# Performance work log

Measured on AMD Instinct MI355X. Metric: run time of the kernel, lower is better.

## Reference

```python
import jax, jax.numpy as jnp
import numpy as np


def setup_inputs() -> dict:
    key = jax.random.key(0)
    k1, k2 = jax.random.split(key)
    # positive inputs -> positive matmul outputs, so log is well-defined
    x = jax.random.uniform(k1, (8, 2048, 1024), dtype=jnp.float32)
    matrix = jax.random.uniform(k2, (1024, 1024), dtype=jnp.float32)
    return {"x": x, "matrix": matrix}


def reference(x, matrix):
    # mm_big: shifted quantized matmul; mm_small: no-shift quantized matmul.
    # In float math both compute the same product (quantization differs only
    # in fixed-point scaling), so we compute it once; XLA would CSE anyway.
    y_big = jnp.einsum('bsk,km->bsm', x, matrix)    # [B,S,M]
    y_small = jnp.einsum('bsk,km->bsm', x, matrix)  # NoShiftMM, same float math

    big = (y_big > 0).astype(x.dtype)   # gt0
    small = 1.0 - big                   # oplus(neg(big)) = 1 + (-big)

    eps = jnp.finfo(x.dtype).tiny
    # AddIdentityTLUT(torch.log): LUT approximation of log; float reference is log.
    z_big = jnp.log(jnp.maximum(y_big, eps)) * big      # lut_big -> mul_big
    z_small = jnp.log(jnp.maximum(y_small, eps)) * small  # lut_small -> mul_small
    return z_big + z_small  # add_output
```

## Files before the change

### kernel.cpp

```cpp
#include <hip/hip_runtime.h>
#include <cstdint>
#include <cstddef>

#define M_GLOB 16384
#define N_GLOB 1024
#define K_GLOB 1024

#define BM 256
#define BN 128
#define BKF 128

typedef unsigned char  u8;
typedef unsigned short u16;
typedef __attribute__((ext_vector_type(4))) float  f32x4;
typedef __attribute__((ext_vector_type(16))) float f32x16;
typedef __attribute__((ext_vector_type(4))) unsigned int  u32x4;
typedef __attribute__((ext_vector_type(2))) unsigned int  u32x2;
typedef __attribute__((ext_vector_type(8))) int  i32x8;
typedef __attribute__((ext_vector_type(8))) __bf16 bf16x8;

typedef const __attribute__((address_space(1))) void* gas1_t;
typedef __attribute__((address_space(3))) void* las3_t;

static __device__ __forceinline__ void load_lds16(const void* g, void* l) {
    __builtin_amdgcn_global_load_lds((gas1_t)g, (las3_t)l, 16, 0, 0);
}

static __device__ __forceinline__ unsigned pack2_bf16(float lo, float hi) {
    unsigned bl = __builtin_bit_cast(unsigned, lo);
    unsigned bh = __builtin_bit_cast(unsigned, hi);
    return (bh & 0xFFFF0000u) | (bl >> 16);
}

static __device__ __forceinline__ unsigned cvt4_fp8(float a, float b, float c, float d) {
    int w = __builtin_amdgcn_cvt_pk_fp8_f32(a, b, 0, false);
    w = __builtin_amdgcn_cvt_pk_fp8_f32(c, d, w, true);
    return (unsigned)w;
}

__global__ __launch_bounds__(256)
void prep_fp8_kernel(const float* __restrict__ A, u8* __restrict__ Ab,
                     const float* __restrict__ B, u8* __restrict__ Bt, int nA) {
    __shared__ float tile[32][33];
    const int tid = threadIdx.x;
    if ((int)blockIdx.x < nA) {
        const size_t i = ((size_t)blockIdx.x * 256 + tid) * 16;
        f32x4 f0 = *(const f32x4*)(A + i);
        f32x4 f1 = *(const f32x4*)(A + i + 4);
        f32x4 f2 = *(const f32x4*)(A + i + 8);
        f32x4 f3 = *(const f32x4*)(A + i + 12);
        u32x4 o;
        o.x = cvt4_fp8(f0.x, f0.y, f0.z, f0.w);
        o.y = cvt4_fp8(f1.x, f1.y, f1.z, f1.w);
        o.z = cvt4_fp8(f2.x, f2.y, f2.z, f2.w);
        o.w = cvt4_fp8(f3.x, f3.y, f3.z, f3.w);
        *(u32x4*)(Ab + i) = o;
    } else {
        const int bid = (int)blockIdx.x - nA;
        const int n0 = (bid & 31) * 32;
        const int k0 = (bid >> 5) * 32;
        const int tx = tid & 31;
        const int ty = tid >> 5;
#pragma unroll
        for (int i = 0; i < 32; i += 8)
            tile[ty + i][tx] = B[(size_t)(k0 + ty + i) * N_GLOB + n0 + tx];
        __syncthreads();
#pragma unroll
        for (int i = 0; i < 32; i += 8) {
            int w = __builtin_amdgcn_cvt_pk_fp8_f32(tile[tx][ty + i], 0.f, 0, false);
            Bt[(size_t)(n0 + ty + i) * K_GLOB + k0 + tx] = (u8)(w & 0xFF);
        }
    }
}

__global__ __launch_bounds__(256, 2)
void gemm_mx_kernel(const u8* __restrict__ A,
                    const u8* __restrict__ Bt,
                    float* __restrict__ C)
{
    __shared__ __attribute__((aligned(16))) char smem[49152];
    float* Cs = (float*)smem;

    const int tid  = threadIdx.x;
    const int wave = tid >> 6;
    const int lane = tid & 63;
    const int wr   = wave >> 1;
    const int wc   = wave & 1;
    const int l32  = lane & 31;
    const int half = lane >> 5;

    const int b    = blockIdx.x;
    const int xcd  = b & 7;
    const int idx  = b >> 3;
    const int m0   = (xcd * 8 + (idx >> 3)) * BM;
    const int n0   = (idx & 7) * BN;

    const int srow = lane >> 3;
    const int sc   = (lane & 7) ^ srow;
    const u8* gA = A  + (size_t)(m0 + srow) * K_GLOB + sc * 16;
    const u8* gB = Bt + (size_t)(n0 + srow) * K_GLOB + sc * 16;

    f32x16 acc[4][2];
#pragma unroll
    for (int i = 0; i < 4; ++i)
#pragma unroll
        for (int j = 0; j < 2; ++j)
#pragma unroll
            for (int r = 0; r < 16; ++r)
                acc[i][j][r] = 0.f;

    const int swz = lane & 7;
    const int scale1 = 0x7F7F7F7F;

    for (int kt = 0; kt < K_GLOB / BKF; ++kt) {
        const size_t k0 = (size_t)kt * BKF;
#pragma unroll
        for (int s = 0; s < 8; ++s) {
            const int rows0 = (s * 4 + wave) * 8;
            load_lds16(gA + (size_t)rows0 * K_GLOB + k0, smem + rows0 * 128);
        }
#pragma unroll
        for (int s = 0; s < 4; ++s) {
            const int rows0 = (s * 4 + wave) * 8;
            load_lds16(gB + (size_t)rows0 * K_GLOB + k0, smem + 32768 + rows0 * 128);
        }
        __syncthreads();

#pragma unroll
        for (int s = 0; s < 2; ++s) {
            const int c0 = s * 4 + half * 2;
            const int p0 = ((c0    ) ^ swz) * 16;
            const int p1 = ((c0 + 1) ^ swz) * 16;
            i32x8 af[4], bf[2];
#pragma unroll
            for (int i = 0; i < 4; ++i) {
                const int row = wr * 128 + i * 32 + l32;
                u32x4 lo = *(const u32x4*)(smem + row * 128 + p0);
                u32x4 hi = *(const u32x4*)(smem + row * 128 + p1);
                af[i][0] = lo.x; af[i][1] = lo.y; af[i][2] = lo.z; af[i][3] = lo.w;
                af[i][4] = hi.x; af[i][5] = hi.y; af[i][6] = hi.z; af[i][7] = hi.w;
            }
#pragma unroll
            for (int j = 0; j < 2; ++j) {
                const int row = wc * 64 + j * 32 + l32;
                u32x4 lo = *(const u32x4*)(smem + 32768 + row * 128 + p0);
                u32x4 hi = *(const u32x4*)(smem + 32768 + row * 128 + p1);
                bf[j][0] = lo.x; bf[j][1] = lo.y; bf[j][2] = lo.z; bf[j][3] = lo.w;
                bf[j][4] = hi.x; bf[j][5] = hi.y; bf[j][6] = hi.z; bf[j][7] = hi.w;
            }
#pragma unroll
            for (int i = 0; i < 4; ++i)
#pragma unroll
                for (int j = 0; j < 2; ++j)
                    acc[i][j] = __builtin_amdgcn_mfma_scale_f32_32x32x64_f8f6f4(
                        af[i], bf[j], acc[i][j],
                        0 , 0 ,
                        0, scale1, 0, scale1);
        }
        __syncthreads();
    }

    const float LN2 = 0.69314718055994530942f;
    const int c4 = tid & 31;
    const int r0 = tid >> 5;
#pragma unroll
    for (int h = 0; h < 4; ++h) {
        __syncthreads();
        if (wr == (h >> 1)) {
#pragma unroll
            for (int ii = 0; ii < 2; ++ii) {
                const int i = (h & 1) * 2 + ii;
#pragma unroll
                for (int j = 0; j < 2; ++j) {
                    const int col = wc * 64 + j * 32 + l32;
#pragma unroll
                    for (int r = 0; r < 16; ++r) {
                        const int row32 = (r & 3) + 8 * (r >> 2) + 4 * half;
                        float v = fmaxf(acc[i][j][r], 1.17549435e-38f);
                        Cs[(ii * 32 + row32) * 132 + col] = __log2f(v) * LN2;
                    }
                }
            }
        }
        __syncthreads();
#pragma unroll
        for (int s2 = 0; s2 < 8; ++s2) {
            const int row = s2 * 8 + r0;
            f32x4 v = *(const f32x4*)&Cs[row * 132 + c4 * 4];
            __builtin_nontemporal_store(v,
                (f32x4*)&C[(size_t)(m0 + h * 64 + row) * N_GLOB + n0 + c4 * 4]);
        }
    }
}

#define FBM 128
#define FBN 128
#define LDK 40
__global__ __launch_bounds__(256)
void logmm_fused_kernel(const float* __restrict__ A,
                        const float* __restrict__ Bf,
                        float* __restrict__ C)
{
    __shared__ u16 As[FBM][LDK];
    __shared__ u16 Bs[FBN][LDK];

    const int tid  = threadIdx.x;
    const int lane = tid & 63;
    const int wave = tid >> 6;
    const int wr   = wave >> 1;
    const int wc   = wave & 1;
    const int quad = lane >> 4;
    const int l16  = lane & 15;

    const int m0 = blockIdx.y * FBM;
    const int n0 = blockIdx.x * FBN;

    f32x4 acc[4][4];
#pragma unroll
    for (int i = 0; i < 4; ++i)
#pragma unroll
        for (int j = 0; j < 4; ++j)
            acc[i][j] = f32x4{0.f, 0.f, 0.f, 0.f};

    const int ga_row = tid >> 2;
    const int ga_c8  = (tid & 3) * 8;
    const int fb_nt = tid >> 3;
    const int fb_kt = tid & 7;

    for (int kt = 0; kt < K_GLOB / 32; ++kt) {
        const int k0 = kt * 32;
#pragma unroll
        for (int s = 0; s < 2; ++s) {
            const int row = ga_row + s * 64;
            const float* src = A + (size_t)(m0 + row) * K_GLOB + k0 + ga_c8;
            f32x4 f0 = *(const f32x4*)src;
            f32x4 f1 = *(const f32x4*)(src + 4);
            u32x4 o;
            o.x = pack2_bf16(f0.x, f0.y);
            o.y = pack2_bf16(f0.z, f0.w);
            o.z = pack2_bf16(f1.x, f1.y);
            o.w = pack2_bf16(f1.z, f1.w);
            *(u32x4*)&As[row][ga_c8] = o;
        }
        {
            f32x4 r0 = *(const f32x4*)(Bf + (size_t)(k0 + fb_kt * 4 + 0) * N_GLOB + n0 + fb_nt * 4);
            f32x4 r1 = *(const f32x4*)(Bf + (size_t)(k0 + fb_kt * 4 + 1) * N_GLOB + n0 + fb_nt * 4);
            f32x4 r2 = *(const f32x4*)(Bf + (size_t)(k0 + fb_kt * 4 + 2) * N_GLOB + n0 + fb_nt * 4);
            f32x4 r3 = *(const f32x4*)(Bf + (size_t)(k0 + fb_kt * 4 + 3) * N_GLOB + n0 + fb_nt * 4);
#pragma unroll
            for (int j = 0; j < 4; ++j) {
                u32x2 o;
                o.x = pack2_bf16(r0[j], r1[j]);
                o.y = pack2_bf16(r2[j], r3[j]);
                *(u32x2*)&Bs[fb_nt * 4 + j][fb_kt * 4] = o;
            }
        }

        __syncthreads();

        bf16x8 af[4], bfr[4];
#pragma unroll
        for (int i = 0; i < 4; ++i)
            af[i] = __builtin_bit_cast(bf16x8, *(const u32x4*)&As[wr * 64 + i * 16 + l16][quad * 8]);
#pragma unroll
        for (int j = 0; j < 4; ++j)
            bfr[j] = __builtin_bit_cast(bf16x8, *(const u32x4*)&Bs[wc * 64 + j * 16 + l16][quad * 8]);

#pragma unroll
        for (int i = 0; i < 4; ++i)
#pragma unroll
            for (int j = 0; j < 4; ++j)
                acc[i][j] = __builtin_amdgcn_mfma_f32_16x16x32_bf16(af[i], bfr[j], acc[i][j], 0, 0, 0);

        __syncthreads();
    }

    const float LN2 = 0.69314718055994530942f;
#pragma unroll
    for (int i = 0; i < 4; ++i) {
#pragma unroll
        for (int j = 0; j < 4; ++j) {
            const int col = n0 + wc * 64 + j * 16 + l16;
#pragma unroll
            for (int r = 0; r < 4; ++r) {
                const int row = m0 + wr * 64 + i * 16 + quad * 4 + r;
                float v = fmaxf(acc[i][j][r], 1.17549435e-38f);
                C[(size_t)row * N_GLOB + col] = __log2f(v) * LN2;
            }
        }
    }
}

extern "C" void kernel_launch(void* const* d_in, const int* in_sizes, int n_in,
                              void* d_out, int out_size, void* d_ws, size_t ws_size,
                              hipStream_t stream) {
    const float* A = (const float*)d_in[0];
    const float* B = (const float*)d_in[1];
    float* C = (float*)d_out;

    const size_t bt_bytes = (size_t)N_GLOB * K_GLOB;
    const size_t ab_bytes = (size_t)M_GLOB * K_GLOB;
    const int nA = (M_GLOB * K_GLOB) / (256 * 16);

    if (ws_size >= bt_bytes + ab_bytes) {
        u8* Bt = (u8*)d_ws;
        u8* Ab = (u8*)d_ws + bt_bytes;
        prep_fp8_kernel<<<nA + 1024, 256, 0, stream>>>(A, Ab, B, Bt, nA);
        gemm_mx_kernel<<<(M_GLOB / BM) * (N_GLOB / BN), 256, 0, stream>>>(Ab, Bt, C);
    } else {
        logmm_fused_kernel<<<dim3(N_GLOB / FBN, M_GLOB / FBM), 256, 0, stream>>>(A, B, C);
    }
}
```

Measured before the change: 132.8 us.

## Prefetch next K tile into registers instead of direct global-to-LDS loads

Replaces the direct global_load_lds copies with register staging: the next K tile is loaded from global memory into registers while the MFMAs for the current tile run, then written to LDS at the top of the next iteration. This is meant to hide global memory latency behind compute, since the old scheme waited on the loads before every tile. The trailing __syncthreads becomes a raw s_barrier with no waitcnt, which relies on the LDS reads having completed before the MFMAs consume them. In exchange it uses more VGPRs for the staging buffers, which may lower occupancy.

```diff
diff --git a/kernel.cpp b/kernel.cpp
--- a/kernel.cpp
+++ b/kernel.cpp
@@ -19,13 +19,6 @@
 typedef __attribute__((ext_vector_type(8))) int  i32x8;
 typedef __attribute__((ext_vector_type(8))) __bf16 bf16x8;
 
-typedef const __attribute__((address_space(1))) void* gas1_t;
-typedef __attribute__((address_space(3))) void* las3_t;
-
-static __device__ __forceinline__ void load_lds16(const void* g, void* l) {
-    __builtin_amdgcn_global_load_lds((gas1_t)g, (las3_t)l, 16, 0, 0);
-}
-
 static __device__ __forceinline__ unsigned pack2_bf16(float lo, float hi) {
     unsigned bl = __builtin_bit_cast(unsigned, lo);
     unsigned bh = __builtin_bit_cast(unsigned, hi);
@@ -36,6 +29,10 @@
     int w = __builtin_amdgcn_cvt_pk_fp8_f32(a, b, 0, false);
     w = __builtin_amdgcn_cvt_pk_fp8_f32(c, d, w, true);
     return (unsigned)w;
+}
+
+static __device__ __forceinline__ void barrier_raw() {
+    asm volatile("s_barrier" ::: "memory");
 }
 
 __global__ __launch_bounds__(256)
@@ -96,7 +93,8 @@
     const int n0   = (idx & 7) * BN;
 
     const int srow = lane >> 3;
-    const int sc   = (lane & 7) ^ srow;
+    const int sp   = lane & 7;
+    const int sc   = sp ^ srow;
     const u8* gA = A  + (size_t)(m0 + srow) * K_GLOB + sc * 16;
     const u8* gB = Bt + (size_t)(n0 + srow) * K_GLOB + sc * 16;
 
@@ -112,19 +110,36 @@
     const int swz = lane & 7;
     const int scale1 = 0x7F7F7F7F;
 
+    u32x4 ra[8], rb[4];
+#pragma unroll
+    for (int s = 0; s < 8; ++s)
+        ra[s] = *(const u32x4*)(gA + (size_t)((s * 4 + wave) * 8) * K_GLOB);
+#pragma unroll
+    for (int s = 0; s < 4; ++s)
+        rb[s] = *(const u32x4*)(gB + (size_t)((s * 4 + wave) * 8) * K_GLOB);
+
     for (int kt = 0; kt < K_GLOB / BKF; ++kt) {
-        const size_t k0 = (size_t)kt * BKF;
 #pragma unroll
         for (int s = 0; s < 8; ++s) {
-            const int rows0 = (s * 4 + wave) * 8;
-            load_lds16(gA + (size_t)rows0 * K_GLOB + k0, smem + rows0 * 128);
+            const int row = (s * 4 + wave) * 8 + srow;
+            *(u32x4*)(smem + row * 128 + sp * 16) = ra[s];
         }
 #pragma unroll
         for (int s = 0; s < 4; ++s) {
-            const int rows0 = (s * 4 + wave) * 8;
-            load_lds16(gB + (size_t)rows0 * K_GLOB + k0, smem + 32768 + rows0 * 128);
-        }
-        __syncthreads();
+            const int row = (s * 4 + wave) * 8 + srow;
+            *(u32x4*)(smem + 32768 + row * 128 + sp * 16) = rb[s];
+        }
+        __syncthreads();
+
+        if (kt + 1 < K_GLOB / BKF) {
+            const size_t k1 = (size_t)(kt + 1) * BKF;
+#pragma unroll
+            for (int s = 0; s < 8; ++s)
+                ra[s] = *(const u32x4*)(gA + (size_t)((s * 4 + wave) * 8) * K_GLOB + k1);
+#pragma unroll
+            for (int s = 0; s < 4; ++s)
+                rb[s] = *(const u32x4*)(gB + (size_t)((s * 4 + wave) * 8) * K_GLOB + k1);
+        }
 
 #pragma unroll
         for (int s = 0; s < 2; ++s) {
@@ -157,7 +172,7 @@
                         0 , 0 ,
                         0, scale1, 0, scale1);
         }
-        __syncthreads();
+        barrier_raw();
     }
 
     const float LN2 = 0.69314718055994530942f;
```

Result: no change. 132.1 us (-0.5%).
